# Kernel tuning notes

Measured on AMD Instinct MI355X. Metric: run time of the kernel, lower is better.

Reference implementation:

```python
import jax, jax.numpy as jnp
import numpy as np


def _unfold2d(x, side):
    # x: (B, C, H, W) -> (B, C, out, out, side, side), stride-1 sliding windows
    H = x.shape[2]
    out = H - side + 1
    idx = jnp.arange(out)[:, None] + jnp.arange(side)[None, :]  # (out, side)
    x = x[:, :, idx, :]        # (B, C, out, side, W)
    x = x[:, :, :, :, idx]     # (B, C, out, side, out, side)
    return jnp.transpose(x, (0, 1, 2, 4, 3, 5))  # (B, C, out, out, side, side)


def setup_inputs() -> dict:
    key = jax.random.key(0)
    k1, k2, k3 = jax.random.split(key, 3)
    img, side, num = 128, 5, 25
    out = img - side + 1  # 124
    x = jax.random.normal(k1, (1, 3, img, img), dtype=jnp.float32)
    w = jax.random.normal(k2, (3, out, out, num, side, side), dtype=jnp.float32)
    q = jax.random.normal(k3, (3, out, out, num, side, side), dtype=jnp.float32)
    return {"x": x, "w": w, "q": q}


def reference(x, w, q):
    side = w.shape[-1]
    # patches: (1, 3, out, out, 1, side, side) -- broadcast replaces torch repeat
    p = _unfold2d(x, side)[:, :, :, :, None, :, :]
    y = (jnp.pi + 2.0 * jnp.arctan(10.0 * (p * w - q))) / (2.0 * jnp.pi)
    y = jnp.log(jnp.prod(y + 0.6, axis=6))  # product over last window dim, then log
    y = jnp.sum(y, axis=5)                   # sum over remaining window dim
    return y  # (1, 3, out, out, num)
```

## Files before the change

### kernel.cpp

```cpp
#include <hip/hip_runtime.h>


#define IMG   128
#define OUT   124
#define NUM   25
#define NOUT  (3 * OUT * OUT * NUM)
#define OPB   256

__device__ __forceinline__ float fast_atan(float z) {
    float az  = __builtin_fabsf(z);
    float r   = __builtin_amdgcn_rcpf(az);
    bool  big = az > 1.0f;
    float t   = big ? r : az;
    float s   = t * t;
    float p   =                     -0.01172120f;
    p = __builtin_fmaf(p, s,         0.05265332f);
    p = __builtin_fmaf(p, s,        -0.11643287f);
    p = __builtin_fmaf(p, s,         0.19354346f);
    p = __builtin_fmaf(p, s,        -0.33262347f);
    p = __builtin_fmaf(p, s,         0.99997726f);
    float a = t * p;
    a = big ? (1.57079632679489662f - a) : a;
    return __builtin_copysignf(a, z);
}

__device__ __forceinline__ float4 load4u(const float* p) {
    float4 v;
    __builtin_memcpy(&v, p, sizeof(float4));
    return v;
}

__global__ __launch_bounds__(OPB) void dendrite_kernel(
    const float* __restrict__ x,
    const float* __restrict__ w,
    const float* __restrict__ q,
    float* __restrict__ out)
{
    const int o = blockIdx.x * OPB + threadIdx.x;
    if (o >= NOUT) return;

    int rem = o / NUM;
    const int j = rem % OUT;  rem /= OUT;
    const int i = rem % OUT;
    const int c = rem / OUT;

    const float* wp = w + (long long)o * NUM;
    const float* qp = q + (long long)o * NUM;
    const float* xp = x + ((long long)c * IMG + i) * IMG + j;

    float wv[NUM], qv[NUM], xv[NUM];
    #pragma unroll
    for (int g = 0; g < 6; ++g) {
        float4 a = load4u(wp + 4 * g);
        wv[4*g+0] = a.x; wv[4*g+1] = a.y; wv[4*g+2] = a.z; wv[4*g+3] = a.w;
    }
    wv[24] = wp[24];
    #pragma unroll
    for (int g = 0; g < 6; ++g) {
        float4 a = load4u(qp + 4 * g);
        qv[4*g+0] = a.x; qv[4*g+1] = a.y; qv[4*g+2] = a.z; qv[4*g+3] = a.w;
    }
    qv[24] = qp[24];
    #pragma unroll
    for (int u = 0; u < 5; ++u) {
        float4 a = load4u(xp + u * IMG);
        xv[5*u+0] = a.x; xv[5*u+1] = a.y; xv[5*u+2] = a.z; xv[5*u+3] = a.w;
        xv[5*u+4] = xp[u * IMG + 4];
    }

    float prod0 = 1.0f, prod1 = 1.0f;
    #pragma unroll
    for (int k = 0; k < NUM; ++k) {
        const float z = 10.0f * __builtin_fmaf(xv[k], wv[k], -qv[k]);
        const float a = fast_atan(z);
        const float term = __builtin_fmaf(a, 0.31830988618379067f, 1.1f);
        if (k & 1) prod1 *= term; else prod0 *= term;
    }
    out[o] = __logf(prod0 * prod1);
}

extern "C" void kernel_launch(void* const* d_in, const int* in_sizes, int n_in,
                              void* d_out, int out_size, void* d_ws, size_t ws_size,
                              hipStream_t stream) {
    const float* x = (const float*)d_in[0];
    const float* w = (const float*)d_in[1];
    const float* q = (const float*)d_in[2];
    float* out = (float*)d_out;

    const int grid = (NOUT + OPB - 1) / OPB;
    dendrite_kernel<<<grid, OPB, 0, stream>>>(x, w, q, out);
}
```

Baseline: 243.4 us.

## Stage w and q tiles into LDS with direct global-to-LDS loads

Each block now copies its contiguous w and q slices into shared memory using 16-byte global_load_lds transfers, which gives fully coalesced global reads in place of the per-thread strided 100-byte vector loads. Threads then read their 25 elements from LDS, where the stride of 25 floats avoids bank conflicts. This adds 51 KB of LDS per block, a barrier, and an explicit vmcnt wait, which may lower occupancy. The old early return is replaced by clamping indices and guarding the compute with tid < nrem.

```diff
diff --git a/kernel.cpp b/kernel.cpp
--- a/kernel.cpp
+++ b/kernel.cpp
@@ -4,7 +4,8 @@
 #define IMG   128
 #define OUT   124
 #define NUM   25
-#define NOUT  (3 * OUT * OUT * NUM)
+#define NPATCH (3 * OUT * OUT)
+#define NOUT  (NPATCH * NUM)
 #define OPB   256
 
 __device__ __forceinline__ float fast_atan(float z) {
@@ -24,10 +25,11 @@
     return __builtin_copysignf(a, z);
 }
 
-__device__ __forceinline__ float4 load4u(const float* p) {
-    float4 v;
-    __builtin_memcpy(&v, p, sizeof(float4));
-    return v;
+__device__ __forceinline__ void copy16_lds(float* l, const float* g) {
+    __builtin_amdgcn_global_load_lds(
+        (const __attribute__((address_space(1))) unsigned int*)g,
+        (__attribute__((address_space(3))) unsigned int*)l,
+        16 , 0 , 0 );
 }
 
 __global__ __launch_bounds__(OPB) void dendrite_kernel(
@@ -36,47 +38,64 @@
     const float* __restrict__ q,
     float* __restrict__ out)
 {
-    const int o = blockIdx.x * OPB + threadIdx.x;
-    if (o >= NOUT) return;
+    __shared__ float w_lds[OPB * NUM];
+    __shared__ float q_lds[OPB * NUM];
 
-    int rem = o / NUM;
+    const int tid = threadIdx.x;
+    const int wvb = tid & ~63;
+    const long long o_base = (long long)blockIdx.x * OPB;
+    const int nrem = min(OPB, (int)(NOUT - o_base));
+    const int lim4 = (nrem * NUM) >> 2;
+
+    const float* wsrc = w + o_base * NUM;
+    const float* qsrc = q + o_base * NUM;
+
+    #pragma unroll
+    for (int r = 0; r < 7; ++r) {
+        const int idx4 = r * OPB + tid;
+        if (idx4 < lim4)
+            copy16_lds(&w_lds[(r * OPB + wvb) * 4], wsrc + idx4 * 4);
+    }
+    #pragma unroll
+    for (int r = 0; r < 7; ++r) {
+        const int idx4 = r * OPB + tid;
+        if (idx4 < lim4)
+            copy16_lds(&q_lds[(r * OPB + wvb) * 4], qsrc + idx4 * 4);
+    }
+
+    const int o  = (int)o_base + tid;
+    const int oc = min(o, NOUT - 1);
+    int rem = oc / NUM;
     const int j = rem % OUT;  rem /= OUT;
     const int i = rem % OUT;
     const int c = rem / OUT;
-
-    const float* wp = w + (long long)o * NUM;
-    const float* qp = q + (long long)o * NUM;
     const float* xp = x + ((long long)c * IMG + i) * IMG + j;
 
-    float wv[NUM], qv[NUM], xv[NUM];
-    #pragma unroll
-    for (int g = 0; g < 6; ++g) {
-        float4 a = load4u(wp + 4 * g);
-        wv[4*g+0] = a.x; wv[4*g+1] = a.y; wv[4*g+2] = a.z; wv[4*g+3] = a.w;
-    }
-    wv[24] = wp[24];
-    #pragma unroll
-    for (int g = 0; g < 6; ++g) {
-        float4 a = load4u(qp + 4 * g);
-        qv[4*g+0] = a.x; qv[4*g+1] = a.y; qv[4*g+2] = a.z; qv[4*g+3] = a.w;
-    }
-    qv[24] = qp[24];
+    float xv[NUM];
     #pragma unroll
     for (int u = 0; u < 5; ++u) {
-        float4 a = load4u(xp + u * IMG);
+        float4 a;
+        __builtin_memcpy(&a, xp + u * IMG, sizeof(float4));
         xv[5*u+0] = a.x; xv[5*u+1] = a.y; xv[5*u+2] = a.z; xv[5*u+3] = a.w;
         xv[5*u+4] = xp[u * IMG + 4];
     }
 
-    float prod0 = 1.0f, prod1 = 1.0f;
-    #pragma unroll
-    for (int k = 0; k < NUM; ++k) {
-        const float z = 10.0f * __builtin_fmaf(xv[k], wv[k], -qv[k]);
-        const float a = fast_atan(z);
-        const float term = __builtin_fmaf(a, 0.31830988618379067f, 1.1f);
-        if (k & 1) prod1 *= term; else prod0 *= term;
+    asm volatile("s_waitcnt vmcnt(0)" ::: "memory");
+    __syncthreads();
+
+    if (tid < nrem) {
+        const float* wl = &w_lds[tid * NUM];
+        const float* ql = &q_lds[tid * NUM];
+        float prod0 = 1.0f, prod1 = 1.0f;
+        #pragma unroll
+        for (int k = 0; k < NUM; ++k) {
+            const float z = 10.0f * __builtin_fmaf(xv[k], wl[k], -ql[k]);
+            const float a = fast_atan(z);
+            const float term = __builtin_fmaf(a, 0.31830988618379067f, 1.1f);
+            if (k & 1) prod1 *= term; else prod0 *= term;
+        }
+        out[o] = __logf(prod0 * prod1);
     }
-    out[o] = __logf(prod0 * prod1);
 }
 
 extern "C" void kernel_launch(void* const* d_in, const int* in_sizes, int n_in,
```

After: 242.8 us. Within noise of the previous version (-0.2%).
